# Performance work log

Hardware: AMD Instinct MI355X
Metric: run time of the kernel (lower is better)

## Reference

```python
import jax, jax.numpy as jnp
import numpy as np

N = 4096          # total nodes
G = 8             # graphs in batch
M_PER = N // G    # nodes per graph (contiguous batch ids)
DEG = 8           # random out-edges per node before symmetrization (~16 after)


def setup_inputs() -> dict:
    rng = np.random.default_rng(0)
    A = np.zeros((N, N), dtype=np.float32)
    for g in range(G):
        lo = g * M_PER
        u = rng.integers(lo, lo + M_PER, size=M_PER * DEG)
        v = rng.integers(lo, lo + M_PER, size=M_PER * DEG)
        A[u, v] = 1.0
        ring = np.arange(lo, lo + M_PER)           # guarantee no isolated nodes
        A[ring, np.roll(ring, -1)] = 1.0
    A = np.maximum(A, A.T)                          # undirected (symmetric)
    np.fill_diagonal(A, 0.0)                        # no self loops
    batch = np.repeat(np.arange(G), M_PER).astype(np.int64)
    return {"A": jnp.asarray(A), "batch": jnp.asarray(batch), "num_graphs": G}


def _netsimile_node_features(A):
    # Vectorized form of the per-node ego-network loop.
    # Row n of M1 is the boolean mask of the 1-hop egonet {n} U N(n);
    # B = M1 @ A counts, for each (n, v), edges from ego1(n) into v, so
    # M2 = M1 | (B > 0) is the 2-hop egonet mask. All loop statistics become
    # row reductions of these matrices.
    n = A.shape[0]
    deg = A.sum(axis=1)                                  # [N] feat0: degree
    deg_safe = jnp.maximum(deg, 1.0)
    f0 = deg
    f2 = jnp.where(deg > 0, (A @ deg) / deg_safe, 0.0)   # scatter_mean(deg[col], row)

    eye = jnp.eye(n, dtype=A.dtype)
    M1 = jnp.maximum(A, eye)                             # [N,N] 1-hop ego masks
    B = M1 @ A                                           # [N,N] one-step reach counts
    f4_raw = (B * M1).sum(axis=1)                        # directed edges inside ego1
    M2 = jnp.maximum(M1, (B > 0).astype(A.dtype))        # [N,N] 2-hop ego masks
    f5 = M2 @ deg - 2.0 * f4_raw                         # sum(mask2[row]) - 2*feat4 (incl. post-loop -=)
    f6 = M2.sum(axis=1) - deg - 1.0                      # |ego2| - deg - 1

    denom = jnp.where(deg > 1, deg * (deg - 1.0), 1.0)
    f1 = jnp.where(deg > 1, (f4_raw - deg) / denom, 0.0)  # clustering coeff
    # undirected graph corrections (data.is_undirected() is True)
    f1 = f1 * 2.0
    f4 = f4_raw / 2.0
    f3 = jnp.where(deg > 0, (A @ f1) / deg_safe, 0.0)     # scatter_mean(f1[col], row)
    return jnp.stack([f0, f1, f2, f3, f4, f5, f6], axis=1)  # [N,7]


def reference(A, batch, num_graphs):
    feat = _netsimile_node_features(A)                   # [N,7]
    n, F = feat.shape
    m = n // num_graphs                                  # equal-size contiguous graphs
    xg = feat.reshape(num_graphs, m, F)                  # batch ids are sorted blocks
    mean = xg.mean(axis=1)                               # [G,7]
    c = xg - mean[:, None, :]
    m2 = (c ** 2).mean(axis=1)
    m3 = (c ** 3).mean(axis=1)
    m4 = (c ** 4).mean(axis=1)
    # torch.median returns the LOWER middle element for even counts
    median = jnp.sort(xg, axis=1)[:, (m - 1) // 2, :]
    eps = jnp.float32(1e-4)
    skew = m3 / jnp.maximum(m2 ** 1.5, eps)
    kurt = m4 / jnp.maximum(m2 ** 2, eps)
    return jnp.hstack([mean, median, jnp.sqrt(m2), skew, kurt])  # [G,35]
```

## Files before the change

### kernel.cpp

```cpp
#include <hip/hip_runtime.h>
#include <stdint.h>

typedef unsigned long long u64;

#define NNODE 4096
#define NG    8
#define M     512
#define W     8

#define OFF_MASK 0
#define OFF_DEG  (262144)
#define OFF_FEAT (262144 + 16384)

__global__ __launch_bounds__(256) void k_pack(const float* __restrict__ A,
                                              u64* __restrict__ gmask,
                                              float* __restrict__ gdeg) {
    int row  = (blockIdx.x << 2) + (threadIdx.x >> 6);
    int lane = threadIdx.x & 63;
    int lo   = (row >> 9) << 9;
    const float* rowp = A + (size_t)row * NNODE + lo;
    float4 a = *(const float4*)(rowp + lane * 8);
    float4 b = *(const float4*)(rowp + lane * 8 + 4);
    unsigned int byte =
        (a.x != 0.f ? 1u : 0u) | (a.y != 0.f ? 2u : 0u) |
        (a.z != 0.f ? 4u : 0u) | (a.w != 0.f ? 8u : 0u) |
        (b.x != 0.f ? 16u : 0u) | (b.y != 0.f ? 32u : 0u) |
        (b.z != 0.f ? 64u : 0u) | (b.w != 0.f ? 128u : 0u);
    ((unsigned char*)gmask)[(size_t)row * 64 + lane] = (unsigned char)byte;
    int c = __popc(byte);
#pragma unroll
    for (int off = 32; off; off >>= 1) c += __shfl_down(c, off, 64);
    if (lane == 0) gdeg[row] = (float)c;
}

static __device__ __forceinline__ u64 shfl_xor_u64(u64 v, int mask) {
    return ((u64)(unsigned)__shfl_xor((int)(v >> 32), mask, 64) << 32) |
           (u64)(unsigned)__shfl_xor((int)(v & 0xffffffffu), mask, 64);
}

__global__ __launch_bounds__(128) void k_feat(const u64* __restrict__ gmask,
                                              const float* __restrict__ gdeg,
                                              float* __restrict__ featg) {
    int g = blockIdx.x >> 6, chunk = blockIdx.x & 63;
    int t = threadIdx.x;
    __shared__ u64 smT[W * M];
    __shared__ float sdeg[M];
    __shared__ u64 planes[9][W];

    const ulonglong2* gm2 = (const ulonglong2*)(gmask + (size_t)g * M * W);
#pragma unroll
    for (int it = 0; it < 16; it++) {
        int idx = t + (it << 7);
        ulonglong2 v = gm2[idx];
        int u = idx >> 2, w2 = (idx & 3) << 1;
        smT[w2 * M + u]       = v.x;
        smT[(w2 + 1) * M + u] = v.y;
    }
    for (int i = t; i < M; i += 128) sdeg[i] = gdeg[g * M + i];
    __syncthreads();

    int wv = t >> 6, lane = t & 63;
    for (int w = wv; w < W; w += 2) {
        int d = (int)sdeg[(w << 6) + lane];
#pragma unroll
        for (int k = 0; k < 9; k++) {
            u64 bal = __ballot(((d >> k) & 1) != 0);
            if (lane == 0) planes[k][w] = bal;
        }
    }
    __syncthreads();

    int nl = t >> 4, q = t & 15;
    int n  = (chunk << 3) + nl;

    u64 m1[W];
#pragma unroll
    for (int ww = 0; ww < W; ww++) m1[ww] = smT[ww * M + n];
    m1[n >> 6] |= 1ull << (n & 63);

    u64 reach[W];
#pragma unroll
    for (int ww = 0; ww < W; ww++) reach[ww] = 0ull;

    int w = q >> 1, h = q & 1;
    u64 myw = smT[w * M + n];
    if (w == (n >> 6)) myw |= 1ull << (n & 63);
    unsigned int bits = h ? (unsigned int)(myw >> 32) : (unsigned int)myw;
    int base = (w << 6) + (h << 5);

    int f4 = 0;
    while (bits) {
        int b = __ffs(bits) - 1;
        bits &= bits - 1;
        int u = base + b;
#pragma unroll
        for (int w2 = 0; w2 < W; w2++) {
            u64 r = smT[w2 * M + u];
            reach[w2] |= r;
            f4 += __popcll(r & m1[w2]);
        }
    }

    u64 s4[4];
#pragma unroll
    for (int i = 0; i < 4; i++) {
        u64 keep = (q & 1) ? reach[i + 4] : reach[i];
        u64 send = (q & 1) ? reach[i]     : reach[i + 4];
        s4[i] = keep | shfl_xor_u64(send, 1);
    }
    u64 s2[2];
#pragma unroll
    for (int i = 0; i < 2; i++) {
        u64 keep = (q & 2) ? s4[i + 2] : s4[i];
        u64 send = (q & 2) ? s4[i]     : s4[i + 2];
        s2[i] = keep | shfl_xor_u64(send, 2);
    }
    u64 s1;
    {
        u64 keep = (q & 4) ? s2[1] : s2[0];
        u64 send = (q & 4) ? s2[0] : s2[1];
        s1 = keep | shfl_xor_u64(send, 4);
    }
    u64 rfin = s1 | shfl_xor_u64(s1, 8);
    int wq = ((q & 1) << 2) | (q & 2) | ((q >> 2) & 1);

    u64 aw  = smT[wq * M + n];
    u64 m1w = aw;
    if (wq == (n >> 6)) m1w |= 1ull << (n & 63);
    u64 m2m = m1w | rfin;

    int f5f6 = 0, f2p = 0;
    if (q < 8) {
        int acc = __popcll(m2m) << 20;
#pragma unroll
        for (int k = 0; k < 9; k++) acc += __popcll(m2m & planes[k][wq]) << k;
        f5f6 = acc;
    } else {
        int acc = 0;
#pragma unroll
        for (int k = 0; k < 9; k++) acc += __popcll(aw & planes[k][wq]) << k;
        f2p = acc;
    }

#pragma unroll
    for (int mk = 1; mk <= 8; mk <<= 1) {
        f4   += __shfl_xor(f4,   mk, 64);
        f5f6 += __shfl_xor(f5f6, mk, 64);
        f2p  += __shfl_xor(f2p,  mk, 64);
    }

    if (q == 0) {
        int f5i = f5f6 & 0xFFFFF;
        int f6c = f5f6 >> 20;
        float deg = sdeg[n];
        float f4raw = (float)f4;
        float f1 = (deg > 1.f) ? 2.f * (f4raw - deg) / (deg * (deg - 1.f)) : 0.f;
        float* fb = featg + (size_t)g * 7 * M;
        fb[0 * M + n] = deg;
        fb[1 * M + n] = f1;
        fb[2 * M + n] = (deg > 0.f) ? (float)f2p / deg : 0.f;
        fb[4 * M + n] = f4raw * 0.5f;
        fb[5 * M + n] = (float)f5i - 2.f * f4raw;
        fb[6 * M + n] = (float)f6c - deg - 1.f;
    }
}

__global__ __launch_bounds__(256) void k_stats(const float* __restrict__ featg,
                                               const u64* __restrict__ gmask,
                                               const float* __restrict__ gdeg,
                                               float* __restrict__ out) {
    int blk = blockIdx.x;
    int gf = blk >> 1, half = blk & 1;
    int g = gf / 7, f = gf % 7;
    int t = threadIdx.x;
    __shared__ __align__(16) float sv[M];
    __shared__ float f1s[M];
    __shared__ double rsum[4], r2[4], r3[4], r4[4];
    __shared__ double smean;

    if (f == 3) {
        f1s[t]       = featg[((size_t)g * 7 + 1) * M + t];
        f1s[t + 256] = featg[((size_t)g * 7 + 1) * M + t + 256];
        __syncthreads();
#pragma unroll
        for (int hh = 0; hh < 2; hh++) {
            int n = t + (hh << 8);
            const u64* mrow = gmask + ((size_t)g * M + n) * W;
            float sum = 0.f;
#pragma unroll
            for (int w = 0; w < W; w++) {
                u64 bits = mrow[w];
                while (bits) {
                    int b = __ffsll(bits) - 1;
                    bits &= bits - 1;
                    sum += f1s[(w << 6) + b];
                }
            }
            float deg = gdeg[g * M + n];
            sv[n] = (deg > 0.f) ? sum / deg : 0.f;
        }
    } else {
        sv[t]       = featg[(size_t)gf * M + t];
        sv[t + 256] = featg[(size_t)gf * M + t + 256];
    }
    __syncthreads();

    int wv = t >> 6, lane = t & 63;
    if (half == 0) {
        double s = (double)sv[t] + (double)sv[t + 256];
#pragma unroll
        for (int off = 32; off; off >>= 1) s += __shfl_xor(s, off, 64);
        if (lane == 0) rsum[wv] = s;
        __syncthreads();
        if (t == 0) smean = (rsum[0] + rsum[1] + rsum[2] + rsum[3]) * (1.0 / 512.0);
        __syncthreads();
        double mean = smean;
        double c1 = (double)sv[t] - mean, c2v = (double)sv[t + 256] - mean;
        double a2 = c1 * c1, b2 = c2v * c2v;
        double p2 = a2 + b2, p3 = a2 * c1 + b2 * c2v, p4 = a2 * a2 + b2 * b2;
#pragma unroll
        for (int off = 32; off; off >>= 1) {
            p2 += __shfl_xor(p2, off, 64);
            p3 += __shfl_xor(p3, off, 64);
            p4 += __shfl_xor(p4, off, 64);
        }
        if (lane == 0) { r2[wv] = p2; r3[wv] = p3; r4[wv] = p4; }
        __syncthreads();
        if (t == 0) {
            double m2 = (r2[0] + r2[1] + r2[2] + r2[3]) * (1.0 / 512.0);
            double m3 = (r3[0] + r3[1] + r3[2] + r3[3]) * (1.0 / 512.0);
            double m4 = (r4[0] + r4[1] + r4[2] + r4[3]) * (1.0 / 512.0);
            double sd = sqrt(m2);
            double den3 = m2 * sd;  if (den3 < 1e-4) den3 = 1e-4;
            double den4 = m2 * m2;  if (den4 < 1e-4) den4 = 1e-4;
            out[g * 35 + f]      = (float)smean;
            out[g * 35 + 14 + f] = (float)sd;
            out[g * 35 + 21 + f] = (float)(m3 / den3);
            out[g * 35 + 28 + f] = (float)(m4 / den4);
        }
    }

    float cv = sv[half * 256 + t];
    int less = 0, eq = 0;
    for (int j = 0; j < M; j += 4) {
        float4 x = *(const float4*)&sv[j];
        less += (x.x < cv) + (x.y < cv) + (x.z < cv) + (x.w < cv);
        eq   += (x.x == cv) + (x.y == cv) + (x.z == cv) + (x.w == cv);
    }
    if (less <= 255 && less + eq > 255) out[g * 35 + 7 + f] = cv;
}

extern "C" void kernel_launch(void* const* d_in, const int* in_sizes, int n_in,
                              void* d_out, int out_size, void* d_ws, size_t ws_size,
                              hipStream_t stream) {
    const float* A = (const float*)d_in[0];
    float* out = (float*)d_out;
    char* ws = (char*)d_ws;
    u64*   gmask = (u64*)(ws + OFF_MASK);
    float* gdeg  = (float*)(ws + OFF_DEG);
    float* featg = (float*)(ws + OFF_FEAT);

    k_pack <<<NNODE / 4, 256, 0, stream>>>(A, gmask, gdeg);
    k_feat <<<NG * 64,   128, 0, stream>>>(gmask, gdeg, featg);
    k_stats<<<NG * 7 * 2, 256, 0, stream>>>(featg, gmask, gdeg, out);
}
```

Baseline: 111.9 us.

## Fuse pack, feature and stats kernels into one cooperative kernel with grid syncs

Merges the three separate kernels into one cooperative launch of 512 blocks of 128 threads, with grid-wide syncs between the pack, per-node feature and statistics phases. The stats phase reuses the smT shared buffer and splits each (graph, feature) pair across four blocks instead of two. The pack phase is remapped so 16 threads cover a row, each reading 32 floats. The aim is to remove two kernel launch gaps and their inter-kernel overhead, at the cost of grid barrier latency and a requirement that all 512 blocks be co-resident.

New measurement: 237.9 us. 113% more time.

```diff
diff --git a/kernel.cpp b/kernel.cpp
--- a/kernel.cpp
+++ b/kernel.cpp
@@ -1,7 +1,9 @@
 #include <hip/hip_runtime.h>
+#include <hip/hip_cooperative_groups.h>
 #include <stdint.h>
 
 typedef unsigned long long u64;
+namespace cg = cooperative_groups;
 
 #define NNODE 4096
 #define NG    8
@@ -12,242 +14,265 @@
 #define OFF_DEG  (262144)
 #define OFF_FEAT (262144 + 16384)
 
-__global__ __launch_bounds__(256) void k_pack(const float* __restrict__ A,
-                                              u64* __restrict__ gmask,
-                                              float* __restrict__ gdeg) {
-    int row  = (blockIdx.x << 2) + (threadIdx.x >> 6);
-    int lane = threadIdx.x & 63;
-    int lo   = (row >> 9) << 9;
-    const float* rowp = A + (size_t)row * NNODE + lo;
-    float4 a = *(const float4*)(rowp + lane * 8);
-    float4 b = *(const float4*)(rowp + lane * 8 + 4);
-    unsigned int byte =
-        (a.x != 0.f ? 1u : 0u) | (a.y != 0.f ? 2u : 0u) |
-        (a.z != 0.f ? 4u : 0u) | (a.w != 0.f ? 8u : 0u) |
-        (b.x != 0.f ? 16u : 0u) | (b.y != 0.f ? 32u : 0u) |
-        (b.z != 0.f ? 64u : 0u) | (b.w != 0.f ? 128u : 0u);
-    ((unsigned char*)gmask)[(size_t)row * 64 + lane] = (unsigned char)byte;
-    int c = __popc(byte);
-#pragma unroll
-    for (int off = 32; off; off >>= 1) c += __shfl_down(c, off, 64);
-    if (lane == 0) gdeg[row] = (float)c;
-}
-
 static __device__ __forceinline__ u64 shfl_xor_u64(u64 v, int mask) {
     return ((u64)(unsigned)__shfl_xor((int)(v >> 32), mask, 64) << 32) |
            (u64)(unsigned)__shfl_xor((int)(v & 0xffffffffu), mask, 64);
 }
 
-__global__ __launch_bounds__(128) void k_feat(const u64* __restrict__ gmask,
-                                              const float* __restrict__ gdeg,
-                                              float* __restrict__ featg) {
-    int g = blockIdx.x >> 6, chunk = blockIdx.x & 63;
-    int t = threadIdx.x;
-    __shared__ u64 smT[W * M];
+__global__ __launch_bounds__(128) void k_fused(const float* __restrict__ A,
+                                               u64* __restrict__ gmask,
+                                               float* __restrict__ gdeg,
+                                               float* __restrict__ featg,
+                                               float* __restrict__ out) {
+    cg::grid_group grid = cg::this_grid();
+    int blk = blockIdx.x;
+    int t   = threadIdx.x;
+
+    __shared__ __align__(16) u64 smT[W * M];
     __shared__ float sdeg[M];
     __shared__ u64 planes[9][W];
-
-    const ulonglong2* gm2 = (const ulonglong2*)(gmask + (size_t)g * M * W);
-#pragma unroll
-    for (int it = 0; it < 16; it++) {
-        int idx = t + (it << 7);
-        ulonglong2 v = gm2[idx];
-        int u = idx >> 2, w2 = (idx & 3) << 1;
-        smT[w2 * M + u]       = v.x;
-        smT[(w2 + 1) * M + u] = v.y;
-    }
-    for (int i = t; i < M; i += 128) sdeg[i] = gdeg[g * M + i];
-    __syncthreads();
-
-    int wv = t >> 6, lane = t & 63;
-    for (int w = wv; w < W; w += 2) {
-        int d = (int)sdeg[(w << 6) + lane];
-#pragma unroll
-        for (int k = 0; k < 9; k++) {
-            u64 bal = __ballot(((d >> k) & 1) != 0);
-            if (lane == 0) planes[k][w] = bal;
-        }
-    }
-    __syncthreads();
-
-    int nl = t >> 4, q = t & 15;
-    int n  = (chunk << 3) + nl;
-
-    u64 m1[W];
-#pragma unroll
-    for (int ww = 0; ww < W; ww++) m1[ww] = smT[ww * M + n];
-    m1[n >> 6] |= 1ull << (n & 63);
-
-    u64 reach[W];
-#pragma unroll
-    for (int ww = 0; ww < W; ww++) reach[ww] = 0ull;
-
-    int w = q >> 1, h = q & 1;
-    u64 myw = smT[w * M + n];
-    if (w == (n >> 6)) myw |= 1ull << (n & 63);
-    unsigned int bits = h ? (unsigned int)(myw >> 32) : (unsigned int)myw;
-    int base = (w << 6) + (h << 5);
-
-    int f4 = 0;
-    while (bits) {
-        int b = __ffs(bits) - 1;
-        bits &= bits - 1;
-        int u = base + b;
-#pragma unroll
-        for (int w2 = 0; w2 < W; w2++) {
-            u64 r = smT[w2 * M + u];
-            reach[w2] |= r;
-            f4 += __popcll(r & m1[w2]);
-        }
-    }
-
-    u64 s4[4];
-#pragma unroll
-    for (int i = 0; i < 4; i++) {
-        u64 keep = (q & 1) ? reach[i + 4] : reach[i];
-        u64 send = (q & 1) ? reach[i]     : reach[i + 4];
-        s4[i] = keep | shfl_xor_u64(send, 1);
-    }
-    u64 s2[2];
-#pragma unroll
-    for (int i = 0; i < 2; i++) {
-        u64 keep = (q & 2) ? s4[i + 2] : s4[i];
-        u64 send = (q & 2) ? s4[i]     : s4[i + 2];
-        s2[i] = keep | shfl_xor_u64(send, 2);
-    }
-    u64 s1;
-    {
-        u64 keep = (q & 4) ? s2[1] : s2[0];
-        u64 send = (q & 4) ? s2[0] : s2[1];
-        s1 = keep | shfl_xor_u64(send, 4);
-    }
-    u64 rfin = s1 | shfl_xor_u64(s1, 8);
-    int wq = ((q & 1) << 2) | (q & 2) | ((q >> 2) & 1);
-
-    u64 aw  = smT[wq * M + n];
-    u64 m1w = aw;
-    if (wq == (n >> 6)) m1w |= 1ull << (n & 63);
-    u64 m2m = m1w | rfin;
-
-    int f5f6 = 0, f2p = 0;
-    if (q < 8) {
-        int acc = __popcll(m2m) << 20;
-#pragma unroll
-        for (int k = 0; k < 9; k++) acc += __popcll(m2m & planes[k][wq]) << k;
-        f5f6 = acc;
-    } else {
-        int acc = 0;
-#pragma unroll
-        for (int k = 0; k < 9; k++) acc += __popcll(aw & planes[k][wq]) << k;
-        f2p = acc;
-    }
-
-#pragma unroll
-    for (int mk = 1; mk <= 8; mk <<= 1) {
-        f4   += __shfl_xor(f4,   mk, 64);
-        f5f6 += __shfl_xor(f5f6, mk, 64);
-        f2p  += __shfl_xor(f2p,  mk, 64);
-    }
-
-    if (q == 0) {
-        int f5i = f5f6 & 0xFFFFF;
-        int f6c = f5f6 >> 20;
-        float deg = sdeg[n];
-        float f4raw = (float)f4;
-        float f1 = (deg > 1.f) ? 2.f * (f4raw - deg) / (deg * (deg - 1.f)) : 0.f;
-        float* fb = featg + (size_t)g * 7 * M;
-        fb[0 * M + n] = deg;
-        fb[1 * M + n] = f1;
-        fb[2 * M + n] = (deg > 0.f) ? (float)f2p / deg : 0.f;
-        fb[4 * M + n] = f4raw * 0.5f;
-        fb[5 * M + n] = (float)f5i - 2.f * f4raw;
-        fb[6 * M + n] = (float)f6c - deg - 1.f;
-    }
-}
-
-__global__ __launch_bounds__(256) void k_stats(const float* __restrict__ featg,
-                                               const u64* __restrict__ gmask,
-                                               const float* __restrict__ gdeg,
-                                               float* __restrict__ out) {
-    int blk = blockIdx.x;
-    int gf = blk >> 1, half = blk & 1;
-    int g = gf / 7, f = gf % 7;
-    int t = threadIdx.x;
-    __shared__ __align__(16) float sv[M];
-    __shared__ float f1s[M];
     __shared__ double rsum[4], r2[4], r3[4], r4[4];
     __shared__ double smean;
 
-    if (f == 3) {
-        f1s[t]       = featg[((size_t)g * 7 + 1) * M + t];
-        f1s[t + 256] = featg[((size_t)g * 7 + 1) * M + t + 256];
+    {
+        int nl = t >> 4, q = t & 15;
+        int row = (blk << 3) + nl;
+        int lo  = (row >> 9) << 9;
+        const float* rowp = A + (size_t)row * NNODE + lo + (q << 5);
+        unsigned int wbits = 0u;
+#pragma unroll
+        for (int i = 0; i < 8; i++) {
+            float4 a = *(const float4*)(rowp + (i << 2));
+            unsigned int nib =
+                (a.x != 0.f ? 1u : 0u) | (a.y != 0.f ? 2u : 0u) |
+                (a.z != 0.f ? 4u : 0u) | (a.w != 0.f ? 8u : 0u);
+            wbits |= nib << (i << 2);
+        }
+        ((unsigned int*)gmask)[(size_t)row * 16 + q] = wbits;
+        int c = __popc(wbits);
+        c += __shfl_xor(c, 1, 64);
+        c += __shfl_xor(c, 2, 64);
+        c += __shfl_xor(c, 4, 64);
+        c += __shfl_xor(c, 8, 64);
+        if (q == 0) gdeg[row] = (float)c;
+    }
+
+    grid.sync();
+
+    {
+        int g = blk >> 6, chunk = blk & 63;
+
+        const ulonglong2* gm2 = (const ulonglong2*)(gmask + (size_t)g * M * W);
+#pragma unroll
+        for (int it = 0; it < 16; it++) {
+            int idx = t + (it << 7);
+            ulonglong2 v = gm2[idx];
+            int u = idx >> 2, w2 = (idx & 3) << 1;
+            smT[w2 * M + u]       = v.x;
+            smT[(w2 + 1) * M + u] = v.y;
+        }
+        for (int i = t; i < M; i += 128) sdeg[i] = gdeg[g * M + i];
         __syncthreads();
-#pragma unroll
-        for (int hh = 0; hh < 2; hh++) {
-            int n = t + (hh << 8);
-            const u64* mrow = gmask + ((size_t)g * M + n) * W;
-            float sum = 0.f;
-#pragma unroll
-            for (int w = 0; w < W; w++) {
-                u64 bits = mrow[w];
-                while (bits) {
-                    int b = __ffsll(bits) - 1;
-                    bits &= bits - 1;
-                    sum += f1s[(w << 6) + b];
+
+        int wv = t >> 6, lane = t & 63;
+        for (int w = wv; w < W; w += 2) {
+            int d = (int)sdeg[(w << 6) + lane];
+#pragma unroll
+            for (int k = 0; k < 9; k++) {
+                u64 bal = __ballot(((d >> k) & 1) != 0);
+                if (lane == 0) planes[k][w] = bal;
+            }
+        }
+        __syncthreads();
+
+        int nl = t >> 4, q = t & 15;
+        int n  = (chunk << 3) + nl;
+
+        u64 m1[W];
+#pragma unroll
+        for (int ww = 0; ww < W; ww++) m1[ww] = smT[ww * M + n];
+        m1[n >> 6] |= 1ull << (n & 63);
+
+        u64 reach[W];
+#pragma unroll
+        for (int ww = 0; ww < W; ww++) reach[ww] = 0ull;
+
+        int w = q >> 1, h = q & 1;
+        u64 myw = smT[w * M + n];
+        if (w == (n >> 6)) myw |= 1ull << (n & 63);
+        unsigned int bits = h ? (unsigned int)(myw >> 32) : (unsigned int)myw;
+        int base = (w << 6) + (h << 5);
+
+        int f4 = 0;
+        while (bits) {
+            int b = __ffs(bits) - 1;
+            bits &= bits - 1;
+            int u = base + b;
+#pragma unroll
+            for (int w2 = 0; w2 < W; w2++) {
+                u64 r = smT[w2 * M + u];
+                reach[w2] |= r;
+                f4 += __popcll(r & m1[w2]);
+            }
+        }
+
+        u64 s4[4];
+#pragma unroll
+        for (int i = 0; i < 4; i++) {
+            u64 keep = (q & 1) ? reach[i + 4] : reach[i];
+            u64 send = (q & 1) ? reach[i]     : reach[i + 4];
+            s4[i] = keep | shfl_xor_u64(send, 1);
+        }
+        u64 s2[2];
+#pragma unroll
+        for (int i = 0; i < 2; i++) {
+            u64 keep = (q & 2) ? s4[i + 2] : s4[i];
+            u64 send = (q & 2) ? s4[i]     : s4[i + 2];
+            s2[i] = keep | shfl_xor_u64(send, 2);
+        }
+        u64 s1;
+        {
+            u64 keep = (q & 4) ? s2[1] : s2[0];
+            u64 send = (q & 4) ? s2[0] : s2[1];
+            s1 = keep | shfl_xor_u64(send, 4);
+        }
+        u64 rfin = s1 | shfl_xor_u64(s1, 8);
+        int wq = ((q & 1) << 2) | (q & 2) | ((q >> 2) & 1);
+
+        u64 aw  = smT[wq * M + n];
+        u64 m1w = aw;
+        if (wq == (n >> 6)) m1w |= 1ull << (n & 63);
+        u64 m2m = m1w | rfin;
+
+        int f5f6 = 0, f2p = 0;
+        if (q < 8) {
+            int acc = __popcll(m2m) << 20;
+#pragma unroll
+            for (int k = 0; k < 9; k++) acc += __popcll(m2m & planes[k][wq]) << k;
+            f5f6 = acc;
+        } else {
+            int acc = 0;
+#pragma unroll
+            for (int k = 0; k < 9; k++) acc += __popcll(aw & planes[k][wq]) << k;
+            f2p = acc;
+        }
+
+#pragma unroll
+        for (int mk = 1; mk <= 8; mk <<= 1) {
+            f4   += __shfl_xor(f4,   mk, 64);
+            f5f6 += __shfl_xor(f5f6, mk, 64);
+            f2p  += __shfl_xor(f2p,  mk, 64);
+        }
+
+        if (q == 0) {
+            int f5i = f5f6 & 0xFFFFF;
+            int f6c = f5f6 >> 20;
+            float deg = sdeg[n];
+            float f4raw = (float)f4;
+            float f1 = (deg > 1.f) ? 2.f * (f4raw - deg) / (deg * (deg - 1.f)) : 0.f;
+            float* fb = featg + (size_t)g * 7 * M;
+            fb[0 * M + n] = deg;
+            fb[1 * M + n] = f1;
+            fb[2 * M + n] = (deg > 0.f) ? (float)f2p / deg : 0.f;
+            fb[4 * M + n] = f4raw * 0.5f;
+            fb[5 * M + n] = (float)f5i - 2.f * f4raw;
+            fb[6 * M + n] = (float)f6c - deg - 1.f;
+        }
+    }
+
+    grid.sync();
+
+    if (blk < 224) {
+        float* sv  = (float*)smT;
+        float* f1s = (float*)smT + M;
+        int gf = blk >> 2, q4 = blk & 3;
+        int g = gf / 7, f = gf % 7;
+
+        if (f == 3) {
+#pragma unroll
+            for (int i = 0; i < 4; i++)
+                f1s[t + (i << 7)] = featg[((size_t)g * 7 + 1) * M + t + (i << 7)];
+            __syncthreads();
+#pragma unroll
+            for (int i = 0; i < 4; i++) {
+                int n = t + (i << 7);
+                const u64* mrow = gmask + ((size_t)g * M + n) * W;
+                float sum = 0.f;
+#pragma unroll
+                for (int w = 0; w < W; w++) {
+                    u64 bits = mrow[w];
+                    while (bits) {
+                        int b = __ffsll(bits) - 1;
+                        bits &= bits - 1;
+                        sum += f1s[(w << 6) + b];
+                    }
                 }
-            }
-            float deg = gdeg[g * M + n];
-            sv[n] = (deg > 0.f) ? sum / deg : 0.f;
-        }
-    } else {
-        sv[t]       = featg[(size_t)gf * M + t];
-        sv[t + 256] = featg[(size_t)gf * M + t + 256];
+                float dg = gdeg[g * M + n];
+                sv[n] = (dg > 0.f) ? sum / dg : 0.f;
+            }
+        } else {
+#pragma unroll
+            for (int i = 0; i < 4; i++)
+                sv[t + (i << 7)] = featg[(size_t)gf * M + t + (i << 7)];
+        }
+        __syncthreads();
+
+        int lane = t & 63, wv = t >> 6;
+        if (q4 == 0) {
+            double sA = (double)sv[t] + (double)sv[t + 256];
+            double sB = (double)sv[t + 128] + (double)sv[t + 384];
+#pragma unroll
+            for (int off = 32; off; off >>= 1) sA += __shfl_xor(sA, off, 64);
+#pragma unroll
+            for (int off = 32; off; off >>= 1) sB += __shfl_xor(sB, off, 64);
+            if (lane == 0) { rsum[wv] = sA; rsum[wv + 2] = sB; }
+            __syncthreads();
+            if (t == 0) smean = (rsum[0] + rsum[1] + rsum[2] + rsum[3]) * (1.0 / 512.0);
+            __syncthreads();
+            double mean = smean;
+            double c1 = (double)sv[t] - mean,       c2v = (double)sv[t + 256] - mean;
+            double a2 = c1 * c1, b2 = c2v * c2v;
+            double pA2 = a2 + b2, pA3 = a2 * c1 + b2 * c2v, pA4 = a2 * a2 + b2 * b2;
+            double d1 = (double)sv[t + 128] - mean, d2v = (double)sv[t + 384] - mean;
+            double e2 = d1 * d1, g2 = d2v * d2v;
+            double pB2 = e2 + g2, pB3 = e2 * d1 + g2 * d2v, pB4 = e2 * e2 + g2 * g2;
+#pragma unroll
+            for (int off = 32; off; off >>= 1) {
+                pA2 += __shfl_xor(pA2, off, 64);
+                pA3 += __shfl_xor(pA3, off, 64);
+                pA4 += __shfl_xor(pA4, off, 64);
+                pB2 += __shfl_xor(pB2, off, 64);
+                pB3 += __shfl_xor(pB3, off, 64);
+                pB4 += __shfl_xor(pB4, off, 64);
+            }
+            if (lane == 0) {
+                r2[wv] = pA2; r3[wv] = pA3; r4[wv] = pA4;
+                r2[wv + 2] = pB2; r3[wv + 2] = pB3; r4[wv + 2] = pB4;
+            }
+            __syncthreads();
+            if (t == 0) {
+                double m2 = (r2[0] + r2[1] + r2[2] + r2[3]) * (1.0 / 512.0);
+                double m3 = (r3[0] + r3[1] + r3[2] + r3[3]) * (1.0 / 512.0);
+                double m4 = (r4[0] + r4[1] + r4[2] + r4[3]) * (1.0 / 512.0);
+                double sd = sqrt(m2);
+                double den3 = m2 * sd;  if (den3 < 1e-4) den3 = 1e-4;
+                double den4 = m2 * m2;  if (den4 < 1e-4) den4 = 1e-4;
+                out[g * 35 + f]      = (float)smean;
+                out[g * 35 + 14 + f] = (float)sd;
+                out[g * 35 + 21 + f] = (float)(m3 / den3);
+                out[g * 35 + 28 + f] = (float)(m4 / den4);
+            }
+        }
+
+        float cv = sv[(q4 << 7) + t];
+        int less = 0, eq = 0;
+        for (int j = 0; j < M; j += 4) {
+            float4 x = *(const float4*)&sv[j];
+            less += (x.x < cv) + (x.y < cv) + (x.z < cv) + (x.w < cv);
+            eq   += (x.x == cv) + (x.y == cv) + (x.z == cv) + (x.w == cv);
+        }
+        if (less <= 255 && less + eq > 255) out[g * 35 + 7 + f] = cv;
     }
-    __syncthreads();
-
-    int wv = t >> 6, lane = t & 63;
-    if (half == 0) {
-        double s = (double)sv[t] + (double)sv[t + 256];
-#pragma unroll
-        for (int off = 32; off; off >>= 1) s += __shfl_xor(s, off, 64);
-        if (lane == 0) rsum[wv] = s;
-        __syncthreads();
-        if (t == 0) smean = (rsum[0] + rsum[1] + rsum[2] + rsum[3]) * (1.0 / 512.0);
-        __syncthreads();
-        double mean = smean;
-        double c1 = (double)sv[t] - mean, c2v = (double)sv[t + 256] - mean;
-        double a2 = c1 * c1, b2 = c2v * c2v;
-        double p2 = a2 + b2, p3 = a2 * c1 + b2 * c2v, p4 = a2 * a2 + b2 * b2;
-#pragma unroll
-        for (int off = 32; off; off >>= 1) {
-            p2 += __shfl_xor(p2, off, 64);
-            p3 += __shfl_xor(p3, off, 64);
-            p4 += __shfl_xor(p4, off, 64);
-        }
-        if (lane == 0) { r2[wv] = p2; r3[wv] = p3; r4[wv] = p4; }
-        __syncthreads();
-        if (t == 0) {
-            double m2 = (r2[0] + r2[1] + r2[2] + r2[3]) * (1.0 / 512.0);
-            double m3 = (r3[0] + r3[1] + r3[2] + r3[3]) * (1.0 / 512.0);
-            double m4 = (r4[0] + r4[1] + r4[2] + r4[3]) * (1.0 / 512.0);
-            double sd = sqrt(m2);
-            double den3 = m2 * sd;  if (den3 < 1e-4) den3 = 1e-4;
-            double den4 = m2 * m2;  if (den4 < 1e-4) den4 = 1e-4;
-            out[g * 35 + f]      = (float)smean;
-            out[g * 35 + 14 + f] = (float)sd;
-            out[g * 35 + 21 + f] = (float)(m3 / den3);
-            out[g * 35 + 28 + f] = (float)(m4 / den4);
-        }
-    }
-
-    float cv = sv[half * 256 + t];
-    int less = 0, eq = 0;
-    for (int j = 0; j < M; j += 4) {
-        float4 x = *(const float4*)&sv[j];
-        less += (x.x < cv) + (x.y < cv) + (x.z < cv) + (x.w < cv);
-        eq   += (x.x == cv) + (x.y == cv) + (x.z == cv) + (x.w == cv);
-    }
-    if (less <= 255 && less + eq > 255) out[g * 35 + 7 + f] = cv;
 }
 
 extern "C" void kernel_launch(void* const* d_in, const int* in_sizes, int n_in,
@@ -260,7 +285,8 @@
     float* gdeg  = (float*)(ws + OFF_DEG);
     float* featg = (float*)(ws + OFF_FEAT);
 
-    k_pack <<<NNODE / 4, 256, 0, stream>>>(A, gmask, gdeg);
-    k_feat <<<NG * 64,   128, 0, stream>>>(gmask, gdeg, featg);
-    k_stats<<<NG * 7 * 2, 256, 0, stream>>>(featg, gmask, gdeg, out);
+    void* args[] = { (void*)&A, (void*)&gmask, (void*)&gdeg,
+                     (void*)&featg, (void*)&out };
+    hipLaunchCooperativeKernel(reinterpret_cast<void*>(k_fused),
+                               dim3(NG * 64), dim3(128), args, 0, stream);
 }
```
